# Kernel optimization log

Hardware: AMD Instinct MI355X
Metric: run time of the kernel (lower is better)

Reference implementation:

```python
import jax, jax.numpy as jnp
import numpy as np

SCALE = 0.1    # BinarizeConv2dSDP scale factor
BN_EPS = 1e-5

def _binarize(x):
    # straight-through sign binarization (STE): forward = sign(x), grad = identity
    return x + jax.lax.stop_gradient(jnp.sign(x) - x)

def _bin_conv3x3(x, w, stride=1):
    # binarize activations and weights; per-output-channel weight scaling alpha = mean|w|
    a_b = _binarize(x)
    alpha = jnp.mean(jnp.abs(w), axis=(1, 2, 3))          # [Cout]
    w_b = _binarize(w)
    y = jax.lax.conv_general_dilated(
        a_b, w_b, window_strides=(stride, stride), padding=((1, 1), (1, 1)),
        dimension_numbers=('NCHW', 'OIHW', 'NCHW'))
    return y * (SCALE * alpha)[None, :, None, None]

def _batchnorm(x, gamma, beta):
    mu = jnp.mean(x, axis=(0, 2, 3), keepdims=True)
    var = jnp.var(x, axis=(0, 2, 3), keepdims=True)
    xh = (x - mu) * jax.lax.rsqrt(var + BN_EPS)
    return xh * gamma[None, :, None, None] + beta[None, :, None, None]

def _prelu(x, a):
    return jnp.where(x >= 0, x, a.reshape(()) * x)

def setup_inputs() -> dict:
    key = jax.random.key(0)
    ks = jax.random.split(key, 5)
    B, C, H, W = 64, 256, 28, 28
    return {
        'x': jax.random.normal(ks[0], (B, C, H, W), jnp.float32),
        'conv1_w': jax.random.normal(ks[1], (C, C, 3, 3), jnp.float32) * 0.05,
        'conv2_w': jax.random.normal(ks[2], (C, C, 3, 3), jnp.float32) * 0.05,
        'bn1_gamma': jnp.ones((C,), jnp.float32),
        'bn1_beta': jnp.zeros((C,), jnp.float32),
        'bn2_gamma': jnp.ones((C,), jnp.float32),
        'bn2_beta': jnp.zeros((C,), jnp.float32),
        'prelu1_a': jnp.full((1,), 0.25, jnp.float32),
        'prelu2_a': jnp.full((1,), 0.25, jnp.float32),
    }

def reference(x, conv1_w, conv2_w, bn1_gamma, bn1_beta, bn2_gamma, bn2_beta, prelu1_a, prelu2_a):
    residual = x
    out = _bin_conv3x3(x, conv1_w, stride=1)
    out = _batchnorm(out, bn1_gamma, bn1_beta)
    out = out + residual
    out = _prelu(out, prelu1_a)
    residual = out
    out = _bin_conv3x3(out, conv2_w, stride=1)
    out = _batchnorm(out, bn2_gamma, bn2_beta)
    out = out + residual
    out = _prelu(out, prelu2_a)
    return out
```

## Files before the change

kernel.cpp:

```cpp
#include <hip/hip_runtime.h>
#include <cstdint>

#define NB 64
#define NC 256
#define HW 784
#define NPIX (NB*HW)
#define NELEM ((size_t)NB*NC*HW)

typedef int v4i  __attribute__((ext_vector_type(4)));
typedef int v16i __attribute__((ext_vector_type(16)));

union U16 { signed char b[16]; int4 v; };

__global__ __launch_bounds__(256) void alpha_k(
    const float* __restrict__ w1, const float* __restrict__ w2,
    float* __restrict__ al1, float* __restrict__ al2) {
  int blk = blockIdx.x;
  int conv = blk >> 8, cout = blk & 255;
  const float* w = (conv ? w2 : w1) + (size_t)cout * 2304;
  int t = threadIdx.x;
  float s = 0.0f;
  for (int i = t; i < 2304; i += 256) s += fabsf(w[i]);
  __shared__ float red[256];
  red[t] = s;
  __syncthreads();
  for (int st = 128; st > 0; st >>= 1) {
    if (t < st) red[t] += red[t + st];
    __syncthreads();
  }
  if (t == 0) (conv ? al2 : al1)[cout] = red[0] / 2304.0f;
}

__global__ __launch_bounds__(256) void wfrag_k(
    const float* __restrict__ w1, const float* __restrict__ w2,
    signed char* __restrict__ Wf1, signed char* __restrict__ Wf2) {
  int bi = blockIdx.x;
  int conv = bi / 72, r = bi % 72, tap = r >> 3, cg = r & 7;
  const float* w = conv ? w2 : w1;
  signed char* Wf = conv ? Wf2 : Wf1;
  int t = threadIdx.x;
  for (int e = t; e < 512; e += 256) {
    int c = e >> 6, lane = e & 63;
    int cout = cg * 32 + (lane & 31);
    int cin0 = c * 32 + (lane >> 5) * 16;
    U16 u;
#pragma unroll
    for (int bb = 0; bb < 16; ++bb) {
      float v = w[((size_t)cout * 256 + cin0 + bb) * 9 + tap];
      u.b[bb] = v > 0.f ? 1 : (v < 0.f ? -1 : 0);
    }
    *(int4*)(Wf + ((((size_t)tap * 8 + c) * 8 + cg) * 64 + lane) * 16) = u.v;
  }
}

__global__ __launch_bounds__(256) void pack_x(
    const float* __restrict__ in, signed char* __restrict__ A) {
  __shared__ float tile[256 * 33];
  int t = threadIdx.x;
  int P0 = blockIdx.x * 32;
  int pl = t & 31, c0 = t >> 5;
  int P = P0 + pl;
  int b = P / HW, hw = P - b * HW;
  size_t base = (size_t)b * (NC * HW) + (size_t)c0 * HW + hw;
#pragma unroll
  for (int i = 0; i < 32; ++i)
    tile[(i * 8 + c0) * 33 + pl] = in[base + (size_t)i * 8 * HW];
  __syncthreads();
  int g = t >> 4, pls = t & 15;
#pragma unroll
  for (int ph = 0; ph < 2; ++ph) {
    int pp = ph * 16 + pls;
    U16 u;
#pragma unroll
    for (int bb = 0; bb < 16; ++bb) {
      float v = tile[(g * 16 + bb) * 33 + pp];
      u.b[bb] = v > 0.f ? 1 : (v < 0.f ? -1 : 0);
    }
    *(int4*)(A + (size_t)(P0 + pp) * 256 + g * 16) = u.v;
  }
}

__global__ __launch_bounds__(256, 3) void conv_mfma(
    const signed char* __restrict__ A, const signed char* __restrict__ Wf,
    short* __restrict__ dotb,
    int* __restrict__ pd, int* __restrict__ pq) {
  __shared__ signed char As[192 * 256 + 256];
  int t = threadIdx.x;
  int lane = t & 63, wid = t >> 6;
  int mblk = blockIdx.x >> 1, nblk = blockIdx.x & 1;
  int p0 = mblk * 128;
  int khalf = lane >> 5;

  {
    const signed char* src = A + (size_t)(p0 - 29) * 256;
#pragma unroll
    for (int i = 0; i < 12; ++i) {
      int off = i * 4096 + t * 16;
      int4 d = *(const int4*)(src + off);
      int r = off >> 8, g = (off >> 4) & 15;
      int gs = g ^ ((r + 3) & 15);
      *(int4*)(As + r * 256 + gs * 16) = d;
    }
    if (t < 16) { int4 z = {0, 0, 0, 0}; *(int4*)(As + 192 * 256 + t * 16) = z; }
  }

  int prow[4], hh[4], ww[4];
#pragma unroll
  for (int i = 0; i < 4; ++i) {
    int p = p0 + i * 32 + (lane & 31);
    prow[i] = p;
    int hw = p % HW;
    hh[i] = hw / 28;
    ww[i] = hw - hh[i] * 28;
  }
  __syncthreads();

  v16i acc0 = {0}, acc1 = {0}, acc2 = {0}, acc3 = {0};
  int cg = nblk * 4 + wid;
  const signed char* wlane = Wf + ((size_t)cg * 64 + lane) * 16;

  for (int ky = 0; ky < 3; ++ky) {
#pragma unroll
    for (int kx = 0; kx < 3; ++kx) {
      int tap = ky * 3 + kx;
      int dlt = (ky - 1) * 28 + (kx - 1);
      int rb[4], kk[4];
#pragma unroll
      for (int i = 0; i < 4; ++i) {
        int hp = hh[i] + ky - 1, wp = ww[i] + kx - 1;
        bool val = ((unsigned)hp < 28u) && ((unsigned)wp < 28u);
        int pr = prow[i] + dlt;
        rb[i] = val ? (pr - (p0 - 29)) * 256 : 192 * 256;
        kk[i] = val ? ((pr & 15) << 4) : 0;
      }
      const signed char* wt = wlane + (size_t)tap * 65536;
#pragma unroll
      for (int c = 0; c < 8; ++c) {
        int gl4 = (c * 2 + khalf) << 4;
        v4i a0 = *(const v4i*)(As + rb[0] + (gl4 ^ kk[0]));
        v4i a1 = *(const v4i*)(As + rb[1] + (gl4 ^ kk[1]));
        v4i a2 = *(const v4i*)(As + rb[2] + (gl4 ^ kk[2]));
        v4i a3 = *(const v4i*)(As + rb[3] + (gl4 ^ kk[3]));
        v4i w = *(const v4i*)(wt + (size_t)c * 8192);
        acc0 = __builtin_amdgcn_mfma_i32_32x32x32_i8(a0, w, acc0, 0, 0, 0);
        acc1 = __builtin_amdgcn_mfma_i32_32x32x32_i8(a1, w, acc1, 0, 0, 0);
        acc2 = __builtin_amdgcn_mfma_i32_32x32x32_i8(a2, w, acc2, 0, 0, 0);
        acc3 = __builtin_amdgcn_mfma_i32_32x32x32_i8(a3, w, acc3, 0, 0, 0);
      }
    }
  }

  int cb = nblk * 128 + wid * 32;
  int s = 0, sq = 0;
#pragma unroll
  for (int q = 0; q < 16; ++q) {
    s  += acc0[q] + acc1[q] + acc2[q] + acc3[q];
    sq += acc0[q] * acc0[q] + acc1[q] * acc1[q] +
          acc2[q] * acc2[q] + acc3[q] * acc3[q];
  }
  s += __shfl_xor(s, 32); sq += __shfl_xor(sq, 32);
  if (lane < 32) {
    pd[mblk * 256 + cb + lane] = s;
    pq[mblk * 256 + cb + lane] = sq;
  }

#pragma unroll
  for (int i = 0; i < 4; ++i) {
    v16i ac = (i == 0) ? acc0 : (i == 1) ? acc1 : (i == 2) ? acc2 : acc3;
    int pr = p0 + i * 32 + 4 * khalf;
#pragma unroll
    for (int q = 0; q < 16; ++q) {
      int row = pr + (q & 3) + 8 * (q >> 2);
      dotb[(size_t)row * 256 + cb + (lane & 31)] = (short)ac[q];
    }
  }
}

__global__ __launch_bounds__(256) void bn_finalize(
    const int* __restrict__ pd, const int* __restrict__ pq,
    const float* __restrict__ alpha, const float* __restrict__ gamma,
    const float* __restrict__ beta, float* __restrict__ scale,
    float* __restrict__ shift) {
  int c = blockIdx.x, t = threadIdx.x;
  long long D = 0, D2 = 0;
  for (int r = t; r < 392; r += 256) {
    D  += (long long)pd[r * 256 + c];
    D2 += (long long)pq[r * 256 + c];
  }
  __shared__ long long rd[256], rq[256];
  rd[t] = D; rq[t] = D2;
  __syncthreads();
  for (int st = 128; st > 0; st >>= 1) {
    if (t < st) { rd[t] += rd[t + st]; rq[t] += rq[t + st]; }
    __syncthreads();
  }
  if (t == 0) {
    float sc = 0.1f * alpha[c];
    const float invN = 1.0f / (float)(NB * HW);
    float md  = (float)rd[0] * invN;
    float ex2 = (float)rq[0] * invN;
    float var = sc * sc * (ex2 - md * md);
    float rs = rsqrtf(var + 1e-5f);
    float g = gamma[c];
    scale[c] = rs * g * sc;
    shift[c] = beta[c] - sc * md * rs * g;
  }
}

__global__ __launch_bounds__(256) void bn_mid(
    const short* __restrict__ dot, const float* __restrict__ x,
    const float* __restrict__ scale, const float* __restrict__ shift,
    const float* __restrict__ pa, float* __restrict__ a1,
    signed char* __restrict__ A) {
  __shared__ short rawd[32 * 264];
  __shared__ float tile[256 * 33];
  __shared__ float ssc[256], ssh[256];
  int t = threadIdx.x;
  int P0 = blockIdx.x * 32;
  ssc[t] = scale[t]; ssh[t] = shift[t];
  float ap = pa[0];
#pragma unroll
  for (int i = 0; i < 4; ++i) {
    int idx = i * 256 + t;
    int pl = idx >> 5, g = idx & 31;
    int4 d = *(const int4*)(dot + (size_t)(P0 + pl) * 256 + g * 8);
    *(int4*)(&rawd[pl * 264 + g * 8]) = d;
  }
  __syncthreads();
  int pl = t & 31, c0 = t >> 5;
  int P = P0 + pl;
  int b = P / HW, hw = P - b * HW;
  size_t base = (size_t)b * (NC * HW) + (size_t)c0 * HW + hw;
#pragma unroll
  for (int i = 0; i < 32; ++i) {
    int c = i * 8 + c0;
    size_t addr = base + (size_t)i * 8 * HW;
    float d = (float)rawd[pl * 264 + c];
    float v = fmaf(d, ssc[c], ssh[c]) + x[addr];
    float o = v >= 0.0f ? v : ap * v;
    a1[addr] = o;
    tile[c * 33 + pl] = o;
  }
  __syncthreads();
  int g = t >> 4, pls = t & 15;
#pragma unroll
  for (int ph = 0; ph < 2; ++ph) {
    int pp = ph * 16 + pls;
    U16 u;
#pragma unroll
    for (int bb = 0; bb < 16; ++bb) {
      float v = tile[(g * 16 + bb) * 33 + pp];
      u.b[bb] = v > 0.f ? 1 : (v < 0.f ? -1 : 0);
    }
    *(int4*)(A + (size_t)(P0 + pp) * 256 + g * 16) = u.v;
  }
}

__global__ __launch_bounds__(256) void bn_fin_apply(
    const short* __restrict__ dot, const float* __restrict__ res,
    const float* __restrict__ scale, const float* __restrict__ shift,
    const float* __restrict__ pa, float* __restrict__ out) {
  __shared__ short rawd[32 * 264];
  __shared__ float ssc[256], ssh[256];
  int t = threadIdx.x;
  int P0 = blockIdx.x * 32;
  ssc[t] = scale[t]; ssh[t] = shift[t];
  float ap = pa[0];
#pragma unroll
  for (int i = 0; i < 4; ++i) {
    int idx = i * 256 + t;
    int pl = idx >> 5, g = idx & 31;
    int4 d = *(const int4*)(dot + (size_t)(P0 + pl) * 256 + g * 8);
    *(int4*)(&rawd[pl * 264 + g * 8]) = d;
  }
  __syncthreads();
  int pl = t & 31, c0 = t >> 5;
  int P = P0 + pl;
  int b = P / HW, hw = P - b * HW;
  size_t base = (size_t)b * (NC * HW) + (size_t)c0 * HW + hw;
#pragma unroll
  for (int i = 0; i < 32; ++i) {
    int c = i * 8 + c0;
    size_t addr = base + (size_t)i * 8 * HW;
    float d = (float)rawd[pl * 264 + c];
    float v = fmaf(d, ssc[c], ssh[c]) + res[addr];
    out[addr] = v >= 0.0f ? v : ap * v;
  }
}

extern "C" void kernel_launch(void* const* d_in, const int* in_sizes, int n_in,
                              void* d_out, int out_size, void* d_ws, size_t ws_size,
                              hipStream_t stream) {
  const float* x   = (const float*)d_in[0];
  const float* w1  = (const float*)d_in[1];
  const float* w2  = (const float*)d_in[2];
  const float* g1  = (const float*)d_in[3];
  const float* b1  = (const float*)d_in[4];
  const float* g2  = (const float*)d_in[5];
  const float* b2  = (const float*)d_in[6];
  const float* pa1 = (const float*)d_in[7];
  const float* pa2 = (const float*)d_in[8];
  float* out = (float*)d_out;

  char* ws = (char*)d_ws;
  short*       dotb = (short*)ws;       ws += (size_t)NPIX * 256 * 2;
  signed char* Abuf = (signed char*)ws; ws += (size_t)NPIX * 256;
  signed char* Wf1  = (signed char*)ws; ws += 589824;
  signed char* Wf2  = (signed char*)ws; ws += 589824;
  int* pd1 = (int*)ws; ws += 392 * 256 * 4;
  int* pq1 = (int*)ws; ws += 392 * 256 * 4;
  int* pd2 = (int*)ws; ws += 392 * 256 * 4;
  int* pq2 = (int*)ws; ws += 392 * 256 * 4;
  float* alpha1 = (float*)ws; ws += 1024;
  float* alpha2 = (float*)ws; ws += 1024;
  float* scale1 = (float*)ws; ws += 1024;
  float* shift1 = (float*)ws; ws += 1024;
  float* scale2 = (float*)ws; ws += 1024;
  float* shift2 = (float*)ws; ws += 1024;

  alpha_k<<<512, 256, 0, stream>>>(w1, w2, alpha1, alpha2);
  wfrag_k<<<144, 256, 0, stream>>>(w1, w2, Wf1, Wf2);
  pack_x<<<NPIX / 32, 256, 0, stream>>>(x, Abuf);

  conv_mfma<<<784, 256, 0, stream>>>(Abuf, Wf1, dotb, pd1, pq1);
  bn_finalize<<<256, 256, 0, stream>>>(pd1, pq1, alpha1, g1, b1, scale1, shift1);
  bn_mid<<<NPIX / 32, 256, 0, stream>>>(dotb, x, scale1, shift1, pa1, out, Abuf);

  conv_mfma<<<784, 256, 0, stream>>>(Abuf, Wf2, dotb, pd2, pq2);
  bn_finalize<<<256, 256, 0, stream>>>(pd2, pq2, alpha2, g2, b2, scale2, shift2);
  bn_fin_apply<<<NPIX / 32, 256, 0, stream>>>(dotb, out, scale2, shift2, pa2, out);
}
```

Baseline: 180.6 us.

## Compute all 256 output channels per conv block with double-buffered fragment prefetch

Each conv block now covers all 256 output channels, with two 32-channel groups per wave, instead of splitting channels across two blocks. This halves the number of blocks and the redundant staging of the input tile into LDS. The tap/channel loop is flattened into 72 software-pipelined steps that prefetch the next A and W fragments while the current MFMAs run. In exchange it uses twice as many accumulator registers (occupancy bound lowered to 2) and launches only 392 blocks, which may underfill the GPU.

```diff
diff --git a/kernel.cpp b/kernel.cpp
--- a/kernel.cpp
+++ b/kernel.cpp
@@ -80,14 +80,14 @@
   }
 }
 
-__global__ __launch_bounds__(256, 3) void conv_mfma(
+__global__ __launch_bounds__(256, 2) void conv_mfma(
     const signed char* __restrict__ A, const signed char* __restrict__ Wf,
     short* __restrict__ dotb,
     int* __restrict__ pd, int* __restrict__ pq) {
   __shared__ signed char As[192 * 256 + 256];
   int t = threadIdx.x;
   int lane = t & 63, wid = t >> 6;
-  int mblk = blockIdx.x >> 1, nblk = blockIdx.x & 1;
+  int mblk = blockIdx.x;
   int p0 = mblk * 128;
   int khalf = lane >> 5;
 
@@ -115,63 +115,102 @@
   }
   __syncthreads();
 
-  v16i acc0 = {0}, acc1 = {0}, acc2 = {0}, acc3 = {0};
-  int cg = nblk * 4 + wid;
-  const signed char* wlane = Wf + ((size_t)cg * 64 + lane) * 16;
-
-  for (int ky = 0; ky < 3; ++ky) {
-#pragma unroll
-    for (int kx = 0; kx < 3; ++kx) {
-      int tap = ky * 3 + kx;
-      int dlt = (ky - 1) * 28 + (kx - 1);
-      int rb[4], kk[4];
+  v16i acc[4][2];
+#pragma unroll
+  for (int i = 0; i < 4; ++i) {
+    v16i z = {0};
+    acc[i][0] = z; acc[i][1] = z;
+  }
+
+  const signed char* wlane = Wf + ((size_t)(wid * 2) * 64 + lane) * 16;
+
+  int rbT[2][4], kkT[2][4];
+#pragma unroll
+  for (int i = 0; i < 4; ++i) {
+    int hp = hh[i] - 1, wp = ww[i] - 1;
+    bool val = ((unsigned)hp < 28u) && ((unsigned)wp < 28u);
+    int pr = prow[i] - 29;
+    rbT[0][i] = val ? (pr - (p0 - 29)) * 256 : 192 * 256;
+    kkT[0][i] = val ? ((pr & 15) << 4) : 0;
+  }
+
+  v4i ab[2][4], wb[2][2];
+#pragma unroll
+  for (int i = 0; i < 4; ++i)
+    ab[0][i] = *(const v4i*)(As + rbT[0][i] + ((khalf << 4) ^ kkT[0][i]));
+  wb[0][0] = *(const v4i*)(wlane);
+  wb[0][1] = *(const v4i*)(wlane + 1024);
+
+#pragma unroll
+  for (int it = 0; it < 72; ++it) {
+    const int cur = it & 1, nxt = cur ^ 1;
+    const int tp = it >> 3, c = it & 7;
+
+    if (c == 7 && tp < 8) {
+      const int tn = tp + 1;
+      const int ky = tn / 3, kx = tn % 3;
+      const int dlt = (ky - 1) * 28 + (kx - 1);
 #pragma unroll
       for (int i = 0; i < 4; ++i) {
         int hp = hh[i] + ky - 1, wp = ww[i] + kx - 1;
         bool val = ((unsigned)hp < 28u) && ((unsigned)wp < 28u);
         int pr = prow[i] + dlt;
-        rb[i] = val ? (pr - (p0 - 29)) * 256 : 192 * 256;
-        kk[i] = val ? ((pr & 15) << 4) : 0;
+        rbT[tn & 1][i] = val ? (pr - (p0 - 29)) * 256 : 192 * 256;
+        kkT[tn & 1][i] = val ? ((pr & 15) << 4) : 0;
       }
-      const signed char* wt = wlane + (size_t)tap * 65536;
-#pragma unroll
-      for (int c = 0; c < 8; ++c) {
-        int gl4 = (c * 2 + khalf) << 4;
-        v4i a0 = *(const v4i*)(As + rb[0] + (gl4 ^ kk[0]));
-        v4i a1 = *(const v4i*)(As + rb[1] + (gl4 ^ kk[1]));
-        v4i a2 = *(const v4i*)(As + rb[2] + (gl4 ^ kk[2]));
-        v4i a3 = *(const v4i*)(As + rb[3] + (gl4 ^ kk[3]));
-        v4i w = *(const v4i*)(wt + (size_t)c * 8192);
-        acc0 = __builtin_amdgcn_mfma_i32_32x32x32_i8(a0, w, acc0, 0, 0, 0);
-        acc1 = __builtin_amdgcn_mfma_i32_32x32x32_i8(a1, w, acc1, 0, 0, 0);
-        acc2 = __builtin_amdgcn_mfma_i32_32x32x32_i8(a2, w, acc2, 0, 0, 0);
-        acc3 = __builtin_amdgcn_mfma_i32_32x32x32_i8(a3, w, acc3, 0, 0, 0);
+    }
+
+    if (it < 71) {
+      const int it1 = it + 1;
+      const int t1 = it1 >> 3, c1 = it1 & 7;
+      const int ts = t1 & 1;
+#pragma unroll
+      for (int i = 0; i < 4; ++i)
+        ab[nxt][i] = *(const v4i*)(
+            As + rbT[ts][i] + ((((c1 * 2 + khalf)) << 4) ^ kkT[ts][i]));
+      const signed char* wt = wlane + (size_t)it1 * 8192;
+      wb[nxt][0] = *(const v4i*)(wt);
+      wb[nxt][1] = *(const v4i*)(wt + 1024);
+    }
+    __builtin_amdgcn_sched_barrier(0);
+
+#pragma unroll
+    for (int i = 0; i < 4; ++i) {
+      acc[i][0] = __builtin_amdgcn_mfma_i32_32x32x32_i8(ab[cur][i], wb[cur][0],
+                                                        acc[i][0], 0, 0, 0);
+      acc[i][1] = __builtin_amdgcn_mfma_i32_32x32x32_i8(ab[cur][i], wb[cur][1],
+                                                        acc[i][1], 0, 0, 0);
+    }
+  }
+
+#pragma unroll
+  for (int j = 0; j < 2; ++j) {
+    int s = 0, sq = 0;
+#pragma unroll
+    for (int i = 0; i < 4; ++i)
+#pragma unroll
+      for (int q = 0; q < 16; ++q) {
+        int v = acc[i][j][q];
+        s += v; sq += v * v;
       }
-    }
-  }
-
-  int cb = nblk * 128 + wid * 32;
-  int s = 0, sq = 0;
-#pragma unroll
-  for (int q = 0; q < 16; ++q) {
-    s  += acc0[q] + acc1[q] + acc2[q] + acc3[q];
-    sq += acc0[q] * acc0[q] + acc1[q] * acc1[q] +
-          acc2[q] * acc2[q] + acc3[q] * acc3[q];
-  }
-  s += __shfl_xor(s, 32); sq += __shfl_xor(sq, 32);
-  if (lane < 32) {
-    pd[mblk * 256 + cb + lane] = s;
-    pq[mblk * 256 + cb + lane] = sq;
-  }
-
-#pragma unroll
-  for (int i = 0; i < 4; ++i) {
-    v16i ac = (i == 0) ? acc0 : (i == 1) ? acc1 : (i == 2) ? acc2 : acc3;
+    s += __shfl_xor(s, 32); sq += __shfl_xor(sq, 32);
+    if (lane < 32) {
+      pd[mblk * 256 + wid * 64 + j * 32 + lane] = s;
+      pq[mblk * 256 + wid * 64 + j * 32 + lane] = sq;
+    }
+  }
+
+#pragma unroll
+  for (int i = 0; i < 4; ++i) {
     int pr = p0 + i * 32 + 4 * khalf;
 #pragma unroll
-    for (int q = 0; q < 16; ++q) {
-      int row = pr + (q & 3) + 8 * (q >> 2);
-      dotb[(size_t)row * 256 + cb + (lane & 31)] = (short)ac[q];
+    for (int j = 0; j < 2; ++j) {
+      int cb = wid * 64 + j * 32;
+#pragma unroll
+      for (int q = 0; q < 16; ++q) {
+        int row = pr + (q & 3) + 8 * (q >> 2);
+        dotb[(size_t)row * 256 + cb + (lane & 31)] = (short)acc[i][j][q];
+      }
     }
   }
 }
@@ -322,11 +361,11 @@
   wfrag_k<<<144, 256, 0, stream>>>(w1, w2, Wf1, Wf2);
   pack_x<<<NPIX / 32, 256, 0, stream>>>(x, Abuf);
 
-  conv_mfma<<<784, 256, 0, stream>>>(Abuf, Wf1, dotb, pd1, pq1);
+  conv_mfma<<<392, 256, 0, stream>>>(Abuf, Wf1, dotb, pd1, pq1);
   bn_finalize<<<256, 256, 0, stream>>>(pd1, pq1, alpha1, g1, b1, scale1, shift1);
   bn_mid<<<NPIX / 32, 256, 0, stream>>>(dotb, x, scale1, shift1, pa1, out, Abuf);
 
-  conv_mfma<<<784, 256, 0, stream>>>(Abuf, Wf2, dotb, pd2, pq2);
+  conv_mfma<<<392, 256, 0, stream>>>(Abuf, Wf2, dotb, pd2, pq2);
   bn_finalize<<<256, 256, 0, stream>>>(pd2, pq2, alpha2, g2, b2, scale2, shift2);
   bn_fin_apply<<<NPIX / 32, 256, 0, stream>>>(dotb, out, scale2, shift2, pa2, out);
 }
```

New measurement: 155.2 us. 14.1% less time.

## Retile binary conv to 64-pixel blocks covering all 256 output channels

Applied to the files above, without the earlier changes.

The implicit-GEMM conv kernel now has each block handle 64 pixels across all 256 output channels, with each wave computing a 2x2 grid of 32x32 MFMA tiles. This replaces 128 pixels by 128 channels, so the halo-padded activation tile in shared memory drops from 192 to 122 rows and occupancy can rise to 4 blocks per CU. The grid stays at 784 blocks, so the BN partial-sum arrays double to 784 rows and bn_finalize reduces over more rows. The intermediate residual is now written to a separate workspace buffer instead of the output tensor, which adds a large workspace allocation.

```diff
diff --git a/kernel.cpp b/kernel.cpp
--- a/kernel.cpp
+++ b/kernel.cpp
@@ -6,6 +6,10 @@
 #define HW 784
 #define NPIX (NB*HW)
 #define NELEM ((size_t)NB*NC*HW)
+
+#define HALO_ROWS 122
+#define A_BYTES (HALO_ROWS*256)
+#define ZERO_OFF A_BYTES
 
 typedef int v4i  __attribute__((ext_vector_type(4)));
 typedef int v16i __attribute__((ext_vector_type(16)));
@@ -80,33 +84,35 @@
   }
 }
 
-__global__ __launch_bounds__(256, 3) void conv_mfma(
+__global__ __launch_bounds__(256, 4) void conv_mfma(
     const signed char* __restrict__ A, const signed char* __restrict__ Wf,
     short* __restrict__ dotb,
     int* __restrict__ pd, int* __restrict__ pq) {
-  __shared__ signed char As[192 * 256 + 256];
+  __shared__ signed char As[A_BYTES + 256];
   int t = threadIdx.x;
   int lane = t & 63, wid = t >> 6;
-  int mblk = blockIdx.x >> 1, nblk = blockIdx.x & 1;
-  int p0 = mblk * 128;
+  int mblk = blockIdx.x;
+  int p0 = mblk * 64;
   int khalf = lane >> 5;
 
   {
     const signed char* src = A + (size_t)(p0 - 29) * 256;
 #pragma unroll
-    for (int i = 0; i < 12; ++i) {
+    for (int i = 0; i < 8; ++i) {
       int off = i * 4096 + t * 16;
-      int4 d = *(const int4*)(src + off);
-      int r = off >> 8, g = (off >> 4) & 15;
-      int gs = g ^ ((r + 3) & 15);
-      *(int4*)(As + r * 256 + gs * 16) = d;
-    }
-    if (t < 16) { int4 z = {0, 0, 0, 0}; *(int4*)(As + 192 * 256 + t * 16) = z; }
-  }
-
-  int prow[4], hh[4], ww[4];
-#pragma unroll
-  for (int i = 0; i < 4; ++i) {
+      if (off < A_BYTES) {
+        int4 d = *(const int4*)(src + off);
+        int r = off >> 8, g = (off >> 4) & 15;
+        int gs = g ^ ((r + 3) & 15);
+        *(int4*)(As + r * 256 + gs * 16) = d;
+      }
+    }
+    if (t < 16) { int4 z = {0, 0, 0, 0}; *(int4*)(As + ZERO_OFF + t * 16) = z; }
+  }
+
+  int prow[2], hh[2], ww[2];
+#pragma unroll
+  for (int i = 0; i < 2; ++i) {
     int p = p0 + i * 32 + (lane & 31);
     prow[i] = p;
     int hw = p % HW;
@@ -115,63 +121,74 @@
   }
   __syncthreads();
 
-  v16i acc0 = {0}, acc1 = {0}, acc2 = {0}, acc3 = {0};
-  int cg = nblk * 4 + wid;
-  const signed char* wlane = Wf + ((size_t)cg * 64 + lane) * 16;
-
-  for (int ky = 0; ky < 3; ++ky) {
-#pragma unroll
-    for (int kx = 0; kx < 3; ++kx) {
-      int tap = ky * 3 + kx;
-      int dlt = (ky - 1) * 28 + (kx - 1);
-      int rb[4], kk[4];
-#pragma unroll
-      for (int i = 0; i < 4; ++i) {
-        int hp = hh[i] + ky - 1, wp = ww[i] + kx - 1;
-        bool val = ((unsigned)hp < 28u) && ((unsigned)wp < 28u);
-        int pr = prow[i] + dlt;
-        rb[i] = val ? (pr - (p0 - 29)) * 256 : 192 * 256;
-        kk[i] = val ? ((pr & 15) << 4) : 0;
+  v16i acc[2][2];
+  {
+    v16i z = {0};
+    acc[0][0] = z; acc[0][1] = z; acc[1][0] = z; acc[1][1] = z;
+  }
+
+  const signed char* wlane = Wf + ((size_t)(wid * 2) * 64 + lane) * 16;
+
+  for (int tap = 0; tap < 9; ++tap) {
+    int ky = (tap >= 3) + (tap >= 6);
+    int kx = tap - 3 * ky;
+    int dlt = (ky - 1) * 28 + (kx - 1);
+    int rb0, rb1, kk0, kk1;
+    {
+      int hp = hh[0] + ky - 1, wp = ww[0] + kx - 1;
+      bool val = ((unsigned)hp < 28u) && ((unsigned)wp < 28u);
+      int pr = prow[0] + dlt;
+      rb0 = val ? (pr - (p0 - 29)) * 256 : ZERO_OFF;
+      kk0 = val ? ((pr & 15) << 4) : 0;
+      hp = hh[1] + ky - 1; wp = ww[1] + kx - 1;
+      val = ((unsigned)hp < 28u) && ((unsigned)wp < 28u);
+      pr = prow[1] + dlt;
+      rb1 = val ? (pr - (p0 - 29)) * 256 : ZERO_OFF;
+      kk1 = val ? ((pr & 15) << 4) : 0;
+    }
+    const signed char* wt = wlane + (size_t)tap * 65536;
+#pragma unroll
+    for (int c = 0; c < 8; ++c) {
+      int gl4 = (c * 2 + khalf) << 4;
+      v4i a0 = *(const v4i*)(As + rb0 + (gl4 ^ kk0));
+      v4i a1 = *(const v4i*)(As + rb1 + (gl4 ^ kk1));
+      v4i w0 = *(const v4i*)(wt + c * 8192);
+      v4i w1 = *(const v4i*)(wt + c * 8192 + 1024);
+      acc[0][0] = __builtin_amdgcn_mfma_i32_32x32x32_i8(a0, w0, acc[0][0], 0, 0, 0);
+      acc[0][1] = __builtin_amdgcn_mfma_i32_32x32x32_i8(a0, w1, acc[0][1], 0, 0, 0);
+      acc[1][0] = __builtin_amdgcn_mfma_i32_32x32x32_i8(a1, w0, acc[1][0], 0, 0, 0);
+      acc[1][1] = __builtin_amdgcn_mfma_i32_32x32x32_i8(a1, w1, acc[1][1], 0, 0, 0);
+    }
+  }
+
+#pragma unroll
+  for (int j = 0; j < 2; ++j) {
+    int s = 0, sq = 0;
+#pragma unroll
+    for (int i = 0; i < 2; ++i)
+#pragma unroll
+      for (int q = 0; q < 16; ++q) {
+        int v = acc[i][j][q];
+        s += v; sq += v * v;
       }
-      const signed char* wt = wlane + (size_t)tap * 65536;
-#pragma unroll
-      for (int c = 0; c < 8; ++c) {
-        int gl4 = (c * 2 + khalf) << 4;
-        v4i a0 = *(const v4i*)(As + rb[0] + (gl4 ^ kk[0]));
-        v4i a1 = *(const v4i*)(As + rb[1] + (gl4 ^ kk[1]));
-        v4i a2 = *(const v4i*)(As + rb[2] + (gl4 ^ kk[2]));
-        v4i a3 = *(const v4i*)(As + rb[3] + (gl4 ^ kk[3]));
-        v4i w = *(const v4i*)(wt + (size_t)c * 8192);
-        acc0 = __builtin_amdgcn_mfma_i32_32x32x32_i8(a0, w, acc0, 0, 0, 0);
-        acc1 = __builtin_amdgcn_mfma_i32_32x32x32_i8(a1, w, acc1, 0, 0, 0);
-        acc2 = __builtin_amdgcn_mfma_i32_32x32x32_i8(a2, w, acc2, 0, 0, 0);
-        acc3 = __builtin_amdgcn_mfma_i32_32x32x32_i8(a3, w, acc3, 0, 0, 0);
+    s += __shfl_xor(s, 32); sq += __shfl_xor(sq, 32);
+    if (lane < 32) {
+      pd[mblk * 256 + wid * 64 + j * 32 + lane] = s;
+      pq[mblk * 256 + wid * 64 + j * 32 + lane] = sq;
+    }
+  }
+
+#pragma unroll
+  for (int i = 0; i < 2; ++i) {
+    int pr = p0 + i * 32 + 4 * khalf;
+#pragma unroll
+    for (int j = 0; j < 2; ++j) {
+      int cb = wid * 64 + j * 32;
+#pragma unroll
+      for (int q = 0; q < 16; ++q) {
+        int row = pr + (q & 3) + 8 * (q >> 2);
+        dotb[(size_t)row * 256 + cb + (lane & 31)] = (short)acc[i][j][q];
       }
-    }
-  }
-
-  int cb = nblk * 128 + wid * 32;
-  int s = 0, sq = 0;
-#pragma unroll
-  for (int q = 0; q < 16; ++q) {
-    s  += acc0[q] + acc1[q] + acc2[q] + acc3[q];
-    sq += acc0[q] * acc0[q] + acc1[q] * acc1[q] +
-          acc2[q] * acc2[q] + acc3[q] * acc3[q];
-  }
-  s += __shfl_xor(s, 32); sq += __shfl_xor(sq, 32);
-  if (lane < 32) {
-    pd[mblk * 256 + cb + lane] = s;
-    pq[mblk * 256 + cb + lane] = sq;
-  }
-
-#pragma unroll
-  for (int i = 0; i < 4; ++i) {
-    v16i ac = (i == 0) ? acc0 : (i == 1) ? acc1 : (i == 2) ? acc2 : acc3;
-    int pr = p0 + i * 32 + 4 * khalf;
-#pragma unroll
-    for (int q = 0; q < 16; ++q) {
-      int row = pr + (q & 3) + 8 * (q >> 2);
-      dotb[(size_t)row * 256 + cb + (lane & 31)] = (short)ac[q];
     }
   }
 }
@@ -183,7 +200,7 @@
     float* __restrict__ shift) {
   int c = blockIdx.x, t = threadIdx.x;
   long long D = 0, D2 = 0;
-  for (int r = t; r < 392; r += 256) {
+  for (int r = t; r < 784; r += 256) {
     D  += (long long)pd[r * 256 + c];
     D2 += (long long)pq[r * 256 + c];
   }
@@ -307,10 +324,11 @@
   signed char* Abuf = (signed char*)ws; ws += (size_t)NPIX * 256;
   signed char* Wf1  = (signed char*)ws; ws += 589824;
   signed char* Wf2  = (signed char*)ws; ws += 589824;
-  int* pd1 = (int*)ws; ws += 392 * 256 * 4;
-  int* pq1 = (int*)ws; ws += 392 * 256 * 4;
-  int* pd2 = (int*)ws; ws += 392 * 256 * 4;
-  int* pq2 = (int*)ws; ws += 392 * 256 * 4;
+  float*       a1   = (float*)ws;       ws += NELEM * 4;
+  int* pd1 = (int*)ws; ws += 784 * 256 * 4;
+  int* pq1 = (int*)ws; ws += 784 * 256 * 4;
+  int* pd2 = (int*)ws; ws += 784 * 256 * 4;
+  int* pq2 = (int*)ws; ws += 784 * 256 * 4;
   float* alpha1 = (float*)ws; ws += 1024;
   float* alpha2 = (float*)ws; ws += 1024;
   float* scale1 = (float*)ws; ws += 1024;
@@ -324,9 +342,9 @@
 
   conv_mfma<<<784, 256, 0, stream>>>(Abuf, Wf1, dotb, pd1, pq1);
   bn_finalize<<<256, 256, 0, stream>>>(pd1, pq1, alpha1, g1, b1, scale1, shift1);
-  bn_mid<<<NPIX / 32, 256, 0, stream>>>(dotb, x, scale1, shift1, pa1, out, Abuf);
+  bn_mid<<<NPIX / 32, 256, 0, stream>>>(dotb, x, scale1, shift1, pa1, a1, Abuf);
 
   conv_mfma<<<784, 256, 0, stream>>>(Abuf, Wf2, dotb, pd2, pq2);
   bn_finalize<<<256, 256, 0, stream>>>(pd2, pq2, alpha2, g2, b2, scale2, shift2);
-  bn_fin_apply<<<NPIX / 32, 256, 0, stream>>>(dotb, out, scale2, shift2, pa2, out);
-}
+  bn_fin_apply<<<NPIX / 32, 256, 0, stream>>>(dotb, a1, scale2, shift2, pa2, out);
+}
```

New measurement: 166.3 us. -7.9%, faster.
